# Kernel tuning notes

Hardware: AMD Instinct MI355X
Metric: run time of the kernel (lower is better)

## Reference

```python
import jax, jax.numpy as jnp
import numpy as np

TAU = 0.2
EPS_NORM = 1e-12  # torch F.normalize eps


def _l2_normalize(x):
    n = jnp.linalg.norm(x, axis=-1, keepdims=True)
    return x / jnp.maximum(n, EPS_NORM)


def setup_inputs() -> dict:
    key = jax.random.key(0)
    k1, k2 = jax.random.split(key)
    seg_emb = jax.random.normal(k1, (131072, 512), dtype=jnp.float32)
    prototypes = jax.random.normal(k2, (64, 512), dtype=jnp.float32) * 0.02
    return {"seg_emb": seg_emb, "prototypes": prototypes}


def reference(seg_emb, prototypes):
    # normalize -> cosine-sim matmul -> temperature scale -> softmax -> weighted proto sum
    p = _l2_normalize(prototypes)          # [K, D]
    z = _l2_normalize(seg_emb)             # [N, D]
    logits = jnp.einsum('nd,kd->nk', z, p) / max(TAU, 1e-06)  # [N, K]
    w = jax.nn.softmax(logits, axis=-1)    # [N, K]
    pattern = jnp.einsum('nk,kd->nd', w, prototypes)           # [N, D]
    return pattern, w, logits
```

## Files before the change

kernel.cpp:

```cpp
#include <hip/hip_runtime.h>
#include <hip/hip_bf16.h>

typedef __attribute__((ext_vector_type(8))) short short8;
typedef __attribute__((ext_vector_type(4))) float f32x4;

#define NPROTO 64
#define DIM    512
#define TAU_INV 5.0f

__device__ __forceinline__ unsigned short f2bf(float f) {
    union { float f; unsigned int u; } v; v.f = f;
    unsigned int r = v.u + 0x7FFFu + ((v.u >> 16) & 1u);
    return (unsigned short)(r >> 16);
}

__global__ void pb_prep(const float* __restrict__ protos,
                        unsigned short* __restrict__ pnorm,
                        unsigned short* __restrict__ protosT) {
    const int k    = blockIdx.x;
    const int lane = threadIdx.x;
    const float* row = protos + k * DIM;
    float x[8];
    float ss = 0.0f;
#pragma unroll
    for (int j = 0; j < 8; ++j) {
        x[j] = row[lane * 8 + j];
        ss += x[j] * x[j];
    }
#pragma unroll
    for (int m = 1; m < 64; m <<= 1) ss += __shfl_xor(ss, m, 64);
    const float s = 1.0f / fmaxf(sqrtf(ss), 1e-12f);
    short8 pn;
#pragma unroll
    for (int j = 0; j < 8; ++j) pn[j] = (short)f2bf(x[j] * s);
    *reinterpret_cast<short8*>(pnorm + k * DIM + lane * 8) = pn;
#pragma unroll
    for (int j = 0; j < 8; ++j)
        protosT[(lane * 8 + j) * NPROTO + k] = f2bf(x[j]);
}

__global__ __launch_bounds__(256, 4) void pb_main(
    const float* __restrict__ seg,
    const unsigned short* __restrict__ pnorm,
    const unsigned short* __restrict__ protosT,
    float* __restrict__ out_pat,
    float* __restrict__ out_w,
    float* __restrict__ out_log) {

    __shared__ unsigned short wbuf_all[4 * 2 * 16 * 64];

    const int wid  = (int)(threadIdx.x >> 6);
    const int lane = (int)(threadIdx.x & 63);
    const int g    = lane >> 4;
    const int r16  = lane & 15;
    const long n0  = ((long)blockIdx.x * 4 + wid) * 32;

    f32x4 acc0[4] = {}, acc1[4] = {};
    float ss0 = 0.0f, ss1 = 0.0f;
    const float* ap0 = seg + (n0 + r16) * DIM + g * 8;
    const float* ap1 = ap0 + 16 * DIM;

    f32x4 a00 = *reinterpret_cast<const f32x4*>(ap0);
    f32x4 a01 = *reinterpret_cast<const f32x4*>(ap0 + 4);
    f32x4 a10 = *reinterpret_cast<const f32x4*>(ap1);
    f32x4 a11 = *reinterpret_cast<const f32x4*>(ap1 + 4);

#pragma unroll
    for (int kt = 0; kt < 16; ++kt) {
        f32x4 n00, n01, n10, n11;
        if (kt < 15) {
            n00 = *reinterpret_cast<const f32x4*>(ap0 + (kt + 1) * 32);
            n01 = *reinterpret_cast<const f32x4*>(ap0 + (kt + 1) * 32 + 4);
            n10 = *reinterpret_cast<const f32x4*>(ap1 + (kt + 1) * 32);
            n11 = *reinterpret_cast<const f32x4*>(ap1 + (kt + 1) * 32 + 4);
        }
        short8 af0, af1;
#pragma unroll
        for (int j = 0; j < 4; ++j) {
            ss0 += a00[j] * a00[j] + a01[j] * a01[j];
            ss1 += a10[j] * a10[j] + a11[j] * a11[j];
            af0[j] = (short)f2bf(a00[j]); af0[j + 4] = (short)f2bf(a01[j]);
            af1[j] = (short)f2bf(a10[j]); af1[j + 4] = (short)f2bf(a11[j]);
        }
        const unsigned short* bbase = pnorm + r16 * DIM + g * 8 + kt * 32;
#pragma unroll
        for (int c = 0; c < 4; ++c) {
            const short8 bf = *reinterpret_cast<const short8*>(bbase + c * 16 * DIM);
            acc0[c] = __builtin_amdgcn_mfma_f32_16x16x32_bf16(af0, bf, acc0[c], 0, 0, 0);
            acc1[c] = __builtin_amdgcn_mfma_f32_16x16x32_bf16(af1, bf, acc1[c], 0, 0, 0);
        }
        if (kt < 15) { a00 = n00; a01 = n01; a10 = n10; a11 = n11; }
    }

    ss0 += __shfl_xor(ss0, 16, 64); ss0 += __shfl_xor(ss0, 32, 64);
    ss1 += __shfl_xor(ss1, 16, 64); ss1 += __shfl_xor(ss1, 32, 64);
    const float sco0 = TAU_INV / fmaxf(sqrtf(ss0), 1e-12f);
    const float sco1 = TAU_INV / fmaxf(sqrtf(ss1), 1e-12f);
    float sc0[4], sc1[4];
#pragma unroll
    for (int q = 0; q < 4; ++q) {
        sc0[q] = __shfl(sco0, g * 4 + q, 64);
        sc1[q] = __shfl(sco1, g * 4 + q, 64);
    }

    float lg0[4][4], lg1[4][4];
#pragma unroll
    for (int c = 0; c < 4; ++c)
#pragma unroll
        for (int q = 0; q < 4; ++q) {
            lg0[c][q] = acc0[c][q] * sc0[q];
            lg1[c][q] = acc1[c][q] * sc1[q];
            out_log[(n0 + g * 4 + q) * NPROTO + c * 16 + r16]      = lg0[c][q];
            out_log[(n0 + 16 + g * 4 + q) * NPROTO + c * 16 + r16] = lg1[c][q];
        }

    float w0[4][4], w1[4][4];
#pragma unroll
    for (int q = 0; q < 4; ++q) {
        float mx0 = fmaxf(fmaxf(lg0[0][q], lg0[1][q]), fmaxf(lg0[2][q], lg0[3][q]));
        float mx1 = fmaxf(fmaxf(lg1[0][q], lg1[1][q]), fmaxf(lg1[2][q], lg1[3][q]));
#pragma unroll
        for (int msk = 1; msk < 16; msk <<= 1) {
            mx0 = fmaxf(mx0, __shfl_xor(mx0, msk, 64));
            mx1 = fmaxf(mx1, __shfl_xor(mx1, msk, 64));
        }
        float e0[4], e1[4], sum0 = 0.0f, sum1 = 0.0f;
#pragma unroll
        for (int c = 0; c < 4; ++c) {
            e0[c] = __expf(lg0[c][q] - mx0); sum0 += e0[c];
            e1[c] = __expf(lg1[c][q] - mx1); sum1 += e1[c];
        }
#pragma unroll
        for (int msk = 1; msk < 16; msk <<= 1) {
            sum0 += __shfl_xor(sum0, msk, 64);
            sum1 += __shfl_xor(sum1, msk, 64);
        }
        const float i0 = 1.0f / sum0, i1 = 1.0f / sum1;
#pragma unroll
        for (int c = 0; c < 4; ++c) { w0[c][q] = e0[c] * i0; w1[c][q] = e1[c] * i1; }
    }

    unsigned short* wb0 = wbuf_all + (wid * 2 + 0) * (16 * 64);
    unsigned short* wb1 = wbuf_all + (wid * 2 + 1) * (16 * 64);
#pragma unroll
    for (int c = 0; c < 4; ++c)
#pragma unroll
        for (int q = 0; q < 4; ++q) {
            out_w[(n0 + g * 4 + q) * NPROTO + c * 16 + r16]      = w0[c][q];
            out_w[(n0 + 16 + g * 4 + q) * NPROTO + c * 16 + r16] = w1[c][q];
            const int row  = g * 4 + q;
            const int col  = c * 16 + r16;
            const int byte = (row * 128 + col * 2) ^ ((row & 7) << 4);
            *reinterpret_cast<unsigned short*>(reinterpret_cast<char*>(wb0) + byte) = f2bf(w0[c][q]);
            *reinterpret_cast<unsigned short*>(reinterpret_cast<char*>(wb1) + byte) = f2bf(w1[c][q]);
        }

    __syncthreads();

    short8 wa[2][2];
    {
        const int row = r16;
        const int b0 = (row * 128 + g * 16)      ^ ((row & 7) << 4);
        const int b1 = (row * 128 + g * 16 + 64) ^ ((row & 7) << 4);
        wa[0][0] = *reinterpret_cast<const short8*>(reinterpret_cast<char*>(wb0) + b0);
        wa[0][1] = *reinterpret_cast<const short8*>(reinterpret_cast<char*>(wb0) + b1);
        wa[1][0] = *reinterpret_cast<const short8*>(reinterpret_cast<char*>(wb1) + b0);
        wa[1][1] = *reinterpret_cast<const short8*>(reinterpret_cast<char*>(wb1) + b1);
    }

#pragma unroll 2
    for (int cp = 0; cp < 32; ++cp) {
        const unsigned short* bp = protosT + (cp * 16 + r16) * NPROTO + g * 8;
        const short8 b0 = *reinterpret_cast<const short8*>(bp);
        const short8 b1 = *reinterpret_cast<const short8*>(bp + 32);
        f32x4 p0 = {}, p1 = {};
        p0 = __builtin_amdgcn_mfma_f32_16x16x32_bf16(wa[0][0], b0, p0, 0, 0, 0);
        p0 = __builtin_amdgcn_mfma_f32_16x16x32_bf16(wa[0][1], b1, p0, 0, 0, 0);
        p1 = __builtin_amdgcn_mfma_f32_16x16x32_bf16(wa[1][0], b0, p1, 0, 0, 0);
        p1 = __builtin_amdgcn_mfma_f32_16x16x32_bf16(wa[1][1], b1, p1, 0, 0, 0);
#pragma unroll
        for (int q = 0; q < 4; ++q) {
            out_pat[(n0 + g * 4 + q) * DIM + cp * 16 + r16]      = p0[q];
            out_pat[(n0 + 16 + g * 4 + q) * DIM + cp * 16 + r16] = p1[q];
        }
    }
}

extern "C" void kernel_launch(void* const* d_in, const int* in_sizes, int n_in,
                              void* d_out, int out_size, void* d_ws, size_t ws_size,
                              hipStream_t stream) {
    const float* seg    = (const float*)d_in[0];
    const float* protos = (const float*)d_in[1];
    const int N = in_sizes[0] / DIM;

    float* out     = (float*)d_out;
    float* out_pat = out;
    float* out_w   = out_pat + (size_t)N * DIM;
    float* out_log = out_w + (size_t)N * NPROTO;

    unsigned short* pnorm   = (unsigned short*)d_ws;
    unsigned short* protosT = pnorm + NPROTO * DIM;

    pb_prep<<<NPROTO, 64, 0, stream>>>(protos, pnorm, protosT);
    pb_main<<<N / 128, 256, 0, stream>>>(seg, pnorm, protosT, out_pat, out_w, out_log);
}
```

Baseline: 167.6 us.

## Stage seg tiles into LDS via async global_load_lds with 4-deep pipeline

Replaces the register double-buffered seg loads with global_load_lds DMA into a 4-slot, XOR-swizzled LDS ring per wave. Prototype B fragments are prefetched three k-steps ahead, with explicit vmcnt waits. The second GEMM's protosT fragments are double-buffered and the loop fully unrolled. The goal is to keep more bytes in flight on this HBM-bound stream; in exchange LDS use grows to about 80KB per block and launch bounds drop to 2 blocks per CU.

New measurement: 169.2 us. Within noise of the previous version (+1.0%).

```diff
diff --git a/kernel.cpp b/kernel.cpp
--- a/kernel.cpp
+++ b/kernel.cpp
@@ -39,7 +39,7 @@
         protosT[(lane * 8 + j) * NPROTO + k] = f2bf(x[j]);
 }
 
-__global__ __launch_bounds__(256, 4) void pb_main(
+__global__ __launch_bounds__(256, 2) void pb_main(
     const float* __restrict__ seg,
     const unsigned short* __restrict__ pnorm,
     const unsigned short* __restrict__ protosT,
@@ -47,6 +47,7 @@
     float* __restrict__ out_w,
     float* __restrict__ out_log) {
 
+    __shared__ char bufA[4 * 4 * 4096];
     __shared__ unsigned short wbuf_all[4 * 2 * 16 * 64];
 
     const int wid  = (int)(threadIdx.x >> 6);
@@ -55,25 +56,56 @@
     const int r16  = lane & 15;
     const long n0  = ((long)blockIdx.x * 4 + wid) * 32;
 
+    const int sr = lane >> 3;
+    const int sj = (lane & 7) ^ (sr & 7);
+    const float* sbase = seg + (n0 + sr) * DIM + sj * 4;
+    char* wavebuf = bufA + wid * 4096;
+
+#define STAGE(KT) do {                                                         \
+    char* _d = wavebuf + ((KT) & 3) * 16384;                                   \
+    const float* _s = sbase + (KT) * 32;                                       \
+    _Pragma("unroll")                                                          \
+    for (int _i = 0; _i < 4; ++_i)                                             \
+        __builtin_amdgcn_global_load_lds(                                      \
+            (const __attribute__((address_space(1))) void*)(_s + _i * 8 * DIM),\
+            (__attribute__((address_space(3))) void*)(_d + _i * 1024),         \
+            16, 0, 0);                                                         \
+} while (0)
+
+    short8 breg[4][4];
+#define BLOAD(KT) do {                                                         \
+    _Pragma("unroll")                                                          \
+    for (int _c = 0; _c < 4; ++_c)                                             \
+        breg[(KT) & 3][_c] = *reinterpret_cast<const short8*>(                 \
+            pnorm + (_c * 16 + r16) * DIM + g * 8 + (KT) * 32);                \
+} while (0)
+
     f32x4 acc0[4] = {}, acc1[4] = {};
     float ss0 = 0.0f, ss1 = 0.0f;
-    const float* ap0 = seg + (n0 + r16) * DIM + g * 8;
-    const float* ap1 = ap0 + 16 * DIM;
-
-    f32x4 a00 = *reinterpret_cast<const f32x4*>(ap0);
-    f32x4 a01 = *reinterpret_cast<const f32x4*>(ap0 + 4);
-    f32x4 a10 = *reinterpret_cast<const f32x4*>(ap1);
-    f32x4 a11 = *reinterpret_cast<const f32x4*>(ap1 + 4);
+
+    STAGE(0); BLOAD(0);
+    STAGE(1); BLOAD(1);
+    STAGE(2); BLOAD(2);
+
+    const int ra  = r16 & 7;
+    const int s0a = ((2 * g)     ^ ra) * 16;
+    const int s0b = ((2 * g + 1) ^ ra) * 16;
 
 #pragma unroll
     for (int kt = 0; kt < 16; ++kt) {
-        f32x4 n00, n01, n10, n11;
-        if (kt < 15) {
-            n00 = *reinterpret_cast<const f32x4*>(ap0 + (kt + 1) * 32);
-            n01 = *reinterpret_cast<const f32x4*>(ap0 + (kt + 1) * 32 + 4);
-            n10 = *reinterpret_cast<const f32x4*>(ap1 + (kt + 1) * 32);
-            n11 = *reinterpret_cast<const f32x4*>(ap1 + (kt + 1) * 32 + 4);
-        }
+        if (kt + 3 < 16) { STAGE(kt + 3); BLOAD(kt + 3); }
+        if (kt <= 12)      asm volatile("s_waitcnt vmcnt(24)" ::: "memory");
+        else if (kt == 13) asm volatile("s_waitcnt vmcnt(16)" ::: "memory");
+        else if (kt == 14) asm volatile("s_waitcnt vmcnt(8)"  ::: "memory");
+        else               asm volatile("s_waitcnt vmcnt(0)"  ::: "memory");
+        __builtin_amdgcn_sched_barrier(0);
+
+        char* sb = wavebuf + (kt & 3) * 16384;
+        const f32x4 a00 = *reinterpret_cast<const f32x4*>(sb + r16 * 128 + s0a);
+        const f32x4 a01 = *reinterpret_cast<const f32x4*>(sb + r16 * 128 + s0b);
+        const f32x4 a10 = *reinterpret_cast<const f32x4*>(sb + (16 + r16) * 128 + s0a);
+        const f32x4 a11 = *reinterpret_cast<const f32x4*>(sb + (16 + r16) * 128 + s0b);
+
         short8 af0, af1;
 #pragma unroll
         for (int j = 0; j < 4; ++j) {
@@ -82,14 +114,11 @@
             af0[j] = (short)f2bf(a00[j]); af0[j + 4] = (short)f2bf(a01[j]);
             af1[j] = (short)f2bf(a10[j]); af1[j + 4] = (short)f2bf(a11[j]);
         }
-        const unsigned short* bbase = pnorm + r16 * DIM + g * 8 + kt * 32;
 #pragma unroll
         for (int c = 0; c < 4; ++c) {
-            const short8 bf = *reinterpret_cast<const short8*>(bbase + c * 16 * DIM);
-            acc0[c] = __builtin_amdgcn_mfma_f32_16x16x32_bf16(af0, bf, acc0[c], 0, 0, 0);
-            acc1[c] = __builtin_amdgcn_mfma_f32_16x16x32_bf16(af1, bf, acc1[c], 0, 0, 0);
-        }
-        if (kt < 15) { a00 = n00; a01 = n01; a10 = n10; a11 = n11; }
+            acc0[c] = __builtin_amdgcn_mfma_f32_16x16x32_bf16(af0, breg[kt & 3][c], acc0[c], 0, 0, 0);
+            acc1[c] = __builtin_amdgcn_mfma_f32_16x16x32_bf16(af1, breg[kt & 3][c], acc1[c], 0, 0, 0);
+        }
     }
 
     ss0 += __shfl_xor(ss0, 16, 64); ss0 += __shfl_xor(ss0, 32, 64);
@@ -168,22 +197,30 @@
         wa[1][1] = *reinterpret_cast<const short8*>(reinterpret_cast<char*>(wb1) + b1);
     }
 
-#pragma unroll 2
+    short8 pbuf[2][2];
+    const unsigned short* btile = protosT + r16 * NPROTO + g * 8;
+    pbuf[0][0] = *reinterpret_cast<const short8*>(btile);
+    pbuf[0][1] = *reinterpret_cast<const short8*>(btile + 32);
+#pragma unroll
     for (int cp = 0; cp < 32; ++cp) {
-        const unsigned short* bp = protosT + (cp * 16 + r16) * NPROTO + g * 8;
-        const short8 b0 = *reinterpret_cast<const short8*>(bp);
-        const short8 b1 = *reinterpret_cast<const short8*>(bp + 32);
+        if (cp < 31) {
+            const unsigned short* bn = btile + (cp + 1) * 16 * NPROTO;
+            pbuf[(cp + 1) & 1][0] = *reinterpret_cast<const short8*>(bn);
+            pbuf[(cp + 1) & 1][1] = *reinterpret_cast<const short8*>(bn + 32);
+        }
         f32x4 p0 = {}, p1 = {};
-        p0 = __builtin_amdgcn_mfma_f32_16x16x32_bf16(wa[0][0], b0, p0, 0, 0, 0);
-        p0 = __builtin_amdgcn_mfma_f32_16x16x32_bf16(wa[0][1], b1, p0, 0, 0, 0);
-        p1 = __builtin_amdgcn_mfma_f32_16x16x32_bf16(wa[1][0], b0, p1, 0, 0, 0);
-        p1 = __builtin_amdgcn_mfma_f32_16x16x32_bf16(wa[1][1], b1, p1, 0, 0, 0);
+        p0 = __builtin_amdgcn_mfma_f32_16x16x32_bf16(wa[0][0], pbuf[cp & 1][0], p0, 0, 0, 0);
+        p0 = __builtin_amdgcn_mfma_f32_16x16x32_bf16(wa[0][1], pbuf[cp & 1][1], p0, 0, 0, 0);
+        p1 = __builtin_amdgcn_mfma_f32_16x16x32_bf16(wa[1][0], pbuf[cp & 1][0], p1, 0, 0, 0);
+        p1 = __builtin_amdgcn_mfma_f32_16x16x32_bf16(wa[1][1], pbuf[cp & 1][1], p1, 0, 0, 0);
 #pragma unroll
         for (int q = 0; q < 4; ++q) {
             out_pat[(n0 + g * 4 + q) * DIM + cp * 16 + r16]      = p0[q];
             out_pat[(n0 + 16 + g * 4 + q) * DIM + cp * 16 + r16] = p1[q];
         }
     }
+#undef STAGE
+#undef BLOAD
 }
 
 extern "C" void kernel_launch(void* const* d_in, const int* in_sizes, int n_in,
```

## Split fused kernel into separate logits/softmax and pattern-matmul kernels

Applied to the files above, without the earlier changes.

Splits the single fused kernel into one kernel that computes logits and softmax weights and a second that reads the fp32 weights back from global memory, converts them to bf16 in LDS and runs the pattern matmul. The pattern kernel also double-buffers the prototype tile loads across iterations. The intent is to make each kernel lighter in registers and phases, improving occupancy and streaming. The cost is an extra kernel launch and an extra global read of the weight matrix.

After: 301.9 us. 1.8x slower.

```diff
diff --git a/kernel.cpp b/kernel.cpp
--- a/kernel.cpp
+++ b/kernel.cpp
@@ -39,15 +39,11 @@
         protosT[(lane * 8 + j) * NPROTO + k] = f2bf(x[j]);
 }
 
-__global__ __launch_bounds__(256, 4) void pb_main(
+__global__ __launch_bounds__(256, 4) void pb_logits(
     const float* __restrict__ seg,
     const unsigned short* __restrict__ pnorm,
-    const unsigned short* __restrict__ protosT,
-    float* __restrict__ out_pat,
     float* __restrict__ out_w,
     float* __restrict__ out_log) {
-
-    __shared__ unsigned short wbuf_all[4 * 2 * 16 * 64];
 
     const int wid  = (int)(threadIdx.x >> 6);
     const int lane = (int)(threadIdx.x & 63);
@@ -140,44 +136,75 @@
         for (int c = 0; c < 4; ++c) { w0[c][q] = e0[c] * i0; w1[c][q] = e1[c] * i1; }
     }
 
-    unsigned short* wb0 = wbuf_all + (wid * 2 + 0) * (16 * 64);
-    unsigned short* wb1 = wbuf_all + (wid * 2 + 1) * (16 * 64);
 #pragma unroll
     for (int c = 0; c < 4; ++c)
 #pragma unroll
         for (int q = 0; q < 4; ++q) {
             out_w[(n0 + g * 4 + q) * NPROTO + c * 16 + r16]      = w0[c][q];
             out_w[(n0 + 16 + g * 4 + q) * NPROTO + c * 16 + r16] = w1[c][q];
-            const int row  = g * 4 + q;
-            const int col  = c * 16 + r16;
-            const int byte = (row * 128 + col * 2) ^ ((row & 7) << 4);
-            *reinterpret_cast<unsigned short*>(reinterpret_cast<char*>(wb0) + byte) = f2bf(w0[c][q]);
-            *reinterpret_cast<unsigned short*>(reinterpret_cast<char*>(wb1) + byte) = f2bf(w1[c][q]);
-        }
-
-    __syncthreads();
+        }
+}
+
+__global__ __launch_bounds__(256, 4) void pb_pattern(
+    const float* __restrict__ w,
+    const unsigned short* __restrict__ protosT,
+    float* __restrict__ out_pat) {
+
+    __shared__ unsigned short wbuf_all[4 * 2 * 16 * 64];
+
+    const int wid  = (int)(threadIdx.x >> 6);
+    const int lane = (int)(threadIdx.x & 63);
+    const int g    = lane >> 4;
+    const int r16  = lane & 15;
+    const long n0  = ((long)blockIdx.x * 4 + wid) * 32;
+
+    unsigned short* wb = wbuf_all + wid * 2048;
+
+    const float* wsrc = w + n0 * NPROTO;
+#pragma unroll
+    for (int i = 0; i < 8; ++i) {
+        const f32x4 v = *reinterpret_cast<const f32x4*>(wsrc + i * 256 + lane * 4);
+        const int row  = i * 4 + (lane >> 4);
+        const int frag = row >> 4;
+        const int r    = row & 15;
+        const int k0   = (lane & 15) * 4;
+        union { unsigned short s[4]; unsigned long long u; } pk;
+#pragma unroll
+        for (int j = 0; j < 4; ++j) pk.s[j] = f2bf(v[j]);
+        const int byte = (r * 128 + k0 * 2) ^ ((r & 7) << 4);
+        *reinterpret_cast<unsigned long long*>(
+            reinterpret_cast<char*>(wb + frag * 1024) + byte) = pk.u;
+    }
 
     short8 wa[2][2];
     {
-        const int row = r16;
-        const int b0 = (row * 128 + g * 16)      ^ ((row & 7) << 4);
-        const int b1 = (row * 128 + g * 16 + 64) ^ ((row & 7) << 4);
-        wa[0][0] = *reinterpret_cast<const short8*>(reinterpret_cast<char*>(wb0) + b0);
-        wa[0][1] = *reinterpret_cast<const short8*>(reinterpret_cast<char*>(wb0) + b1);
-        wa[1][0] = *reinterpret_cast<const short8*>(reinterpret_cast<char*>(wb1) + b0);
-        wa[1][1] = *reinterpret_cast<const short8*>(reinterpret_cast<char*>(wb1) + b1);
-    }
-
-#pragma unroll 2
+        const int b0 = (r16 * 128 + g * 16)      ^ ((r16 & 7) << 4);
+        const int b1 = (r16 * 128 + g * 16 + 64) ^ ((r16 & 7) << 4);
+#pragma unroll
+        for (int f = 0; f < 2; ++f) {
+            wa[f][0] = *reinterpret_cast<const short8*>(
+                reinterpret_cast<char*>(wb + f * 1024) + b0);
+            wa[f][1] = *reinterpret_cast<const short8*>(
+                reinterpret_cast<char*>(wb + f * 1024) + b1);
+        }
+    }
+
+    short8 pbuf[2][2];
+    const unsigned short* btile = protosT + r16 * NPROTO + g * 8;
+    pbuf[0][0] = *reinterpret_cast<const short8*>(btile);
+    pbuf[0][1] = *reinterpret_cast<const short8*>(btile + 32);
+#pragma unroll
     for (int cp = 0; cp < 32; ++cp) {
-        const unsigned short* bp = protosT + (cp * 16 + r16) * NPROTO + g * 8;
-        const short8 b0 = *reinterpret_cast<const short8*>(bp);
-        const short8 b1 = *reinterpret_cast<const short8*>(bp + 32);
+        if (cp < 31) {
+            const unsigned short* bn = btile + (cp + 1) * 16 * NPROTO;
+            pbuf[(cp + 1) & 1][0] = *reinterpret_cast<const short8*>(bn);
+            pbuf[(cp + 1) & 1][1] = *reinterpret_cast<const short8*>(bn + 32);
+        }
         f32x4 p0 = {}, p1 = {};
-        p0 = __builtin_amdgcn_mfma_f32_16x16x32_bf16(wa[0][0], b0, p0, 0, 0, 0);
-        p0 = __builtin_amdgcn_mfma_f32_16x16x32_bf16(wa[0][1], b1, p0, 0, 0, 0);
-        p1 = __builtin_amdgcn_mfma_f32_16x16x32_bf16(wa[1][0], b0, p1, 0, 0, 0);
-        p1 = __builtin_amdgcn_mfma_f32_16x16x32_bf16(wa[1][1], b1, p1, 0, 0, 0);
+        p0 = __builtin_amdgcn_mfma_f32_16x16x32_bf16(wa[0][0], pbuf[cp & 1][0], p0, 0, 0, 0);
+        p0 = __builtin_amdgcn_mfma_f32_16x16x32_bf16(wa[0][1], pbuf[cp & 1][1], p0, 0, 0, 0);
+        p1 = __builtin_amdgcn_mfma_f32_16x16x32_bf16(wa[1][0], pbuf[cp & 1][0], p1, 0, 0, 0);
+        p1 = __builtin_amdgcn_mfma_f32_16x16x32_bf16(wa[1][1], pbuf[cp & 1][1], p1, 0, 0, 0);
 #pragma unroll
         for (int q = 0; q < 4; ++q) {
             out_pat[(n0 + g * 4 + q) * DIM + cp * 16 + r16]      = p0[q];
@@ -202,5 +229,6 @@
     unsigned short* protosT = pnorm + NPROTO * DIM;
 
     pb_prep<<<NPROTO, 64, 0, stream>>>(protos, pnorm, protosT);
-    pb_main<<<N / 128, 256, 0, stream>>>(seg, pnorm, protosT, out_pat, out_w, out_log);
-}
+    pb_logits<<<N / 128, 256, 0, stream>>>(seg, pnorm, out_w, out_log);
+    pb_pattern<<<N / 128, 256, 0, stream>>>(out_w, protosT, out_pat);
+}
```
